# Kernel optimization log

Hardware: AMD Instinct MI355X
Metric: run time of the kernel (lower is better)

## Reference

```python
import jax, jax.numpy as jnp
from jax import lax
import numpy as np

SMOOTH = 1e-4
BN_EPS = 1e-5


def setup_inputs() -> dict:
    key = jax.random.key(0)
    k0, k1, k2, k3 = jax.random.split(key, 4)
    B, C, H, W = 8, 256, 32, 32
    heads, head_dim = 8, 64
    inner = heads * head_dim
    x = jax.random.normal(k0, (B, C, H, W), jnp.float32)
    w_qkv = jax.random.normal(k1, (3 * inner, C, 3, 3), jnp.float32) * 0.02
    head_scale = jax.random.normal(k2, (heads,), jnp.float32)
    w_out = jax.random.normal(k3, (C, inner, 1, 1), jnp.float32) * 0.05
    gamma = jnp.ones((C,), jnp.float32)
    beta = jnp.zeros((C,), jnp.float32)
    return {"x": x, "w_qkv": w_qkv, "head_scale": head_scale,
            "w_out": w_out, "gamma": gamma, "beta": beta}


def _relative_pos_dis(H, W):
    yy, xx = jnp.meshgrid(jnp.arange(H), jnp.arange(W), indexing="ij")
    y = yy.reshape(-1).astype(jnp.float32)
    x = xx.reshape(-1).astype(jnp.float32)
    dy = (y[:, None] - y[None, :]) / H
    dx = (x[:, None] - x[None, :]) / W
    return dy * dy + dx * dx  # [HW, HW]


def reference(x, w_qkv, head_scale, w_out, gamma, beta):
    B, C, H, W = x.shape
    heads = head_scale.shape[0]
    N = H * W
    # qkv 3x3 conv, no bias
    qkv = lax.conv_general_dilated(x, w_qkv, (1, 1), "SAME",
                                   dimension_numbers=("NCHW", "OIHW", "NCHW"))
    inner = qkv.shape[1] // 3
    d = inner // heads
    q, k, v = jnp.split(qkv, 3, axis=1)
    # 'b (g d) h w -> b g (h w) d'
    def resh(t):
        return t.reshape(B, heads, d, N).transpose(0, 1, 3, 2)
    q, k, v = resh(q), resh(k), resh(v)
    # cosine-similarity attention (smoothed)
    attn = jnp.einsum("bgnd,bgmd->bgnm", q, k)
    qn = jnp.sqrt(jnp.sum(q * q, axis=-1) + SMOOTH)  # [B,g,N]
    kn = jnp.sqrt(jnp.sum(k * k, axis=-1) + SMOOTH)
    attn = attn / (qn[:, :, :, None] * kn[:, :, None, :] + SMOOTH)
    # learned per-head Gaussian positional bias
    s = jax.nn.sigmoid(head_scale) * (0.4 - 0.003) + 0.003
    scale_factor = 1.0 / (2.0 * s * s)  # [g]
    dis = _relative_pos_dis(H, W)  # [N,N]
    pb = jnp.exp(-scale_factor[:, None, None] * dis[None, :, :])
    pb = pb / jnp.sum(pb, axis=-1, keepdims=True)
    attn = attn * pb[None]
    out = jnp.einsum("bgnm,bgmd->bgnd", attn, v)
    # 'b g (h w) d -> b (g d) h w'
    out = out.transpose(0, 1, 3, 2).reshape(B, inner, H, W)
    # output projection: 1x1 conv + BatchNorm2d (train-mode batch stats) + ReLU
    out = lax.conv_general_dilated(out, w_out, (1, 1), "VALID",
                                   dimension_numbers=("NCHW", "OIHW", "NCHW"))
    mean = jnp.mean(out, axis=(0, 2, 3))
    var = jnp.mean((out - mean[None, :, None, None]) ** 2, axis=(0, 2, 3))
    out = (out - mean[None, :, None, None]) * (
        gamma[None, :, None, None] * lax.rsqrt(var + BN_EPS)[None, :, None, None]
    ) + beta[None, :, None, None]
    return jax.nn.relu(out)
```

## Files before the change

### kernel.cpp

```cpp
#include <hip/hip_runtime.h>
#include <math.h>

#define SMOOTH 1e-4f
#define BN_EPS 1e-5f

constexpr int Bn = 8;
constexpr int Cc = 256;
constexpr int Nn = 1024;
constexpr int G = 8;
constexpr int INNER = 512;
constexpr int OC = 1536;
constexpr int KK = 2304;

typedef unsigned short u16;
typedef __bf16 bf16x8 __attribute__((ext_vector_type(8)));
typedef float f32x4 __attribute__((ext_vector_type(4)));
typedef unsigned short us8 __attribute__((ext_vector_type(8)));
typedef unsigned short us4 __attribute__((ext_vector_type(4)));

__device__ __forceinline__ u16 f2bf(float f) {
  unsigned int u = __float_as_uint(f);
  unsigned int r = (u + 0x7fffu + ((u >> 16) & 1u)) >> 16;
  return (u16)r;
}
__device__ __forceinline__ float bf2f(u16 u) {
  return __uint_as_float(((unsigned int)u) << 16);
}

__device__ __forceinline__ float waveSum(float v) {
#pragma unroll
  for (int off = 32; off > 0; off >>= 1) v += __shfl_xor(v, off, 64);
  return v;
}

__device__ __forceinline__ void gl16(const u16* g, u16* l) {
  __builtin_amdgcn_global_load_lds(
      (const __attribute__((address_space(1))) unsigned int*)g,
      (__attribute__((address_space(3))) unsigned int*)l, 16, 0, 0);
}

__device__ __forceinline__ bf16x8 ld8(const u16* p) {
  return __builtin_bit_cast(bf16x8, *reinterpret_cast<const us8*>(p));
}

__device__ __forceinline__ void barrier_raw() {
  asm volatile("" ::: "memory");
  __builtin_amdgcn_s_barrier();
  asm volatile("" ::: "memory");
  __builtin_amdgcn_sched_barrier(0);
}

__device__ __forceinline__ bf16x8 ldfrag(const u16* base, int row, int col) {
  int idx = (row * 64 + col) ^ ((row & 7) << 3);
  return ld8(base + idx);
}

__global__ __launch_bounds__(256) void prep_kernel(
    const float* __restrict__ wq, const float* __restrict__ wout,
    const float* __restrict__ x, const float* __restrict__ head_scale,
    u16* __restrict__ wA, u16* __restrict__ wB, u16* __restrict__ xT,
    u16* __restrict__ zpage, float* __restrict__ etab,
    float* __restrict__ idn) {
  __shared__ __align__(16) char smraw[9216];
  const int bid = blockIdx.x;
  const int tid = threadIdx.x;

  if (bid < 1536) {
    float* sw = (float*)smraw;
    const int oc = bid;
    for (int i = tid; i < KK; i += 256) sw[i] = wq[(size_t)oc * KK + i];
    __syncthreads();
#pragma unroll
    for (int j = 0; j < 2; ++j) {
      int c8 = tid + j * 256;
      if (c8 < KK / 8) {
        us8 v;
#pragma unroll
        for (int e = 0; e < 8; ++e) {
          int k = c8 * 8 + e;
          int tap = k >> 8, ic = k & 255;
          v[e] = f2bf(sw[ic * 9 + tap]);
        }
        *reinterpret_cast<us8*>(wA + (size_t)oc * KK + c8 * 8) = v;
      }
    }
  } else if (bid < 1600) {
    const int idx = (bid - 1536) * 256 + tid;
    const float4 a = reinterpret_cast<const float4*>(wout)[idx * 2];
    const float4 b = reinterpret_cast<const float4*>(wout)[idx * 2 + 1];
    us8 v;
    v[0] = f2bf(a.x); v[1] = f2bf(a.y); v[2] = f2bf(a.z); v[3] = f2bf(a.w);
    v[4] = f2bf(b.x); v[5] = f2bf(b.y); v[6] = f2bf(b.z); v[7] = f2bf(b.w);
    reinterpret_cast<us8*>(wB)[idx] = v;
    if (bid == 1536) zpage[tid] = 0;
  } else if (bid < 2112) {
    u16* sxt = (u16*)smraw;
    const int lb = bid - 1600;
    const int b = lb >> 6;
    const int nt = (lb >> 1) & 31;
    const int icc = lb & 1;
    const int n0 = nt * 32;
    const int ic0 = icc * 128;
    const float* xb = x + (size_t)b * Cc * Nn;
    {
      const int px = tid & 31;
      const int ic8 = tid >> 5;
#pragma unroll
      for (int i2 = 0; i2 < 16; ++i2) {
        const int ic = ic8 * 16 + i2;
        sxt[px * 136 + ic] = f2bf(xb[(size_t)(ic0 + ic) * Nn + n0 + px]);
      }
    }
    __syncthreads();
    const int c8 = tid & 7;
    const int px = tid >> 3;
    u16* dst = xT + (((size_t)b * 1024 + n0 + px) * 256) + ic0 + c8 * 8;
#pragma unroll
    for (int c32 = 0; c32 < 2; ++c32)
      *reinterpret_cast<us8*>(dst + c32 * 64) =
          *reinterpret_cast<const us8*>(sxt + px * 136 + c32 * 64 + c8 * 8);
  } else {
    float* et = (float*)smraw;
    float* rsum = (float*)smraw + 64;
    const int g = bid - 2112;
    const float hs = head_scale[g];
    const float sg = 1.f / (1.f + __expf(-hs));
    const float s = sg * (0.4f - 0.003f) + 0.003f;
    const float sf = 1.f / (2.f * s * s);
    if (tid < 64) {
      float v = 0.f;
      if (tid < 63) {
        float d = (float)(tid - 31) * (1.f / 32.f);
        v = __expf(-sf * d * d);
      }
      et[tid] = v;
      etab[g * 64 + tid] = v;
    }
    __syncthreads();
    if (tid < 32) {
      float sum = 0.f;
#pragma unroll
      for (int ym = 0; ym < 32; ++ym) sum += et[tid - ym + 31];
      rsum[tid] = sum;
    }
    __syncthreads();
    for (int i = tid; i < 1024; i += 256)
      idn[g * 1024 + i] = 1.f / (rsum[i >> 5] * rsum[i & 31]);
  }
}

__global__ __launch_bounds__(512, 1) void qkv_gemm_kernel(
    const u16* __restrict__ wA, const u16* __restrict__ xT,
    const u16* __restrict__ zpage, const float* __restrict__ idn,
    u16* __restrict__ qt, u16* __restrict__ ktp, u16* __restrict__ vt) {
  const int tid = threadIdx.x;
  const int lane = tid & 63;
  const int wv = tid >> 6;
  const int wm = wv >> 2, wn = wv & 3;
  const int h = lane >> 4, l15 = lane & 15;
  const int wgid = ((int)blockIdx.x & 7) * 32 + ((int)blockIdx.x >> 3);
  const int bm = wgid & 7;
  const int bn = wgid >> 3;
  const int m0 = bm * 192;

  __shared__ __align__(16) u16 smem[57344];

  const int arow = tid >> 3;
  const int aslot = (tid & 7) ^ (arow & 7);
  const u16* gA0 = wA + (size_t)(m0 + arow) * KK + aslot * 8;
  const int bslot8 = ((tid & 3) ^ (((tid >> 2) & 3) ^ ((tid >> 4) & 3))) * 8;
  const int pimgBase = ((bn & 3) << 8) + (tid >> 2);
  const u16* xTb = xT + (size_t)(bn >> 2) * (1024 * 256);

  auto mkSrc = [&](int tap, int pass) -> const u16* {
    const int dyq = (tap * 11) >> 5;
    const int ddx = tap - 3 * dyq - 1;
    const int ddy = dyq - 1;
    const int pimg = pimgBase + pass * 128;
    const int sx = (pimg & 31) + ddx;
    const int sy = (pimg >> 5) + ddy;
    if (((unsigned)sx < 32u) && ((unsigned)sy < 32u))
      return xTb + (size_t)(pimg + ddx + ddy * 32) * 256 + bslot8;
    return zpage;
  };
  const u16* srcB0 = mkSrc(0, 0);
  const u16* srcB1 = mkSrc(0, 1);
  int koff = 0;

  const int aX = l15 & 7;
  const int bX = (l15 & 3) ^ ((l15 >> 2) & 3);
  const u16* aBase = smem + (wm * 96 + l15) * 64;
  const u16* bBase = smem + 12288 + (wn * 64 + l15) * 32;
  const int slA0 = (h ^ aX) * 8;
  const int slA1 = ((4 + h) ^ aX) * 8;
  const int slB = (h ^ bX) * 8;

  f32x4 acc[6][4];
#pragma unroll
  for (int i = 0; i < 6; ++i)
#pragma unroll
    for (int j = 0; j < 4; ++j) acc[i][j] = (f32x4){0.f, 0.f, 0.f, 0.f};

  auto STAGE_A = [&](int pass, int dbuf, int kti) {
    gl16(gA0 + (size_t)pass * 64 * KK + kti * 64,
         smem + dbuf + pass * 4096 + tid * 8);
  };
  auto STAGE_B = [&](int kap, int pass, int dbuf) {
    gl16((pass ? srcB1 : srcB0) + koff + kap * 32,
         smem + dbuf + 12288 + kap * 8192 + pass * 4096 + tid * 8);
  };

  STAGE_A(0, 0, 0); STAGE_A(1, 0, 0); STAGE_A(2, 0, 0);
  STAGE_B(0, 0, 0); STAGE_B(0, 1, 0);
  STAGE_B(1, 0, 0); STAGE_B(1, 1, 0);
  asm volatile("s_waitcnt vmcnt(2)" ::: "memory");
  barrier_raw();

  bf16x8 af[3], bf[4];
#pragma unroll 1
  for (int kt = 0; kt < 36; ++kt) {
    const int buf = (kt & 1) * 28672;
    const int nbuf = 28672 - buf;
    const bool more = (kt < 35);

    if (more && (kt & 3) == 3) {
      const int ntap = (kt + 1) >> 2;
      srcB0 = mkSrc(ntap, 0);
      srcB1 = mkSrc(ntap, 1);
    }
    koff = ((kt + 1) & 3) << 6;

#pragma unroll
    for (int ni = 0; ni < 4; ++ni) bf[ni] = ld8(bBase + buf + ni * 512 + slB);
#pragma unroll
    for (int q = 0; q < 3; ++q) af[q] = ld8(aBase + buf + q * 1024 + slA0);
    if (more) { STAGE_A(0, nbuf, kt + 1); STAGE_A(1, nbuf, kt + 1); }
    barrier_raw();
    __builtin_amdgcn_s_setprio(1);
#pragma unroll
    for (int q = 0; q < 3; ++q)
#pragma unroll
      for (int ni = 0; ni < 4; ++ni)
        acc[q][ni] = __builtin_amdgcn_mfma_f32_16x16x32_bf16(af[q], bf[ni], acc[q][ni], 0, 0, 0);
    __builtin_amdgcn_s_setprio(0);

#pragma unroll
    for (int q = 0; q < 3; ++q) af[q] = ld8(aBase + buf + (3 + q) * 1024 + slA0);
    if (more) {
      STAGE_A(2, nbuf, kt + 1); STAGE_B(0, 0, nbuf);
      asm volatile("s_waitcnt vmcnt(4)" ::: "memory");
    } else {
      asm volatile("s_waitcnt vmcnt(0)" ::: "memory");
    }
    barrier_raw();
    __builtin_amdgcn_s_setprio(1);
#pragma unroll
    for (int q = 0; q < 3; ++q)
#pragma unroll
      for (int ni = 0; ni < 4; ++ni)
        acc[3 + q][ni] = __builtin_amdgcn_mfma_f32_16x16x32_bf16(af[q], bf[ni], acc[3 + q][ni], 0, 0, 0);
    __builtin_amdgcn_s_setprio(0);

#pragma unroll
    for (int ni = 0; ni < 4; ++ni) bf[ni] = ld8(bBase + buf + 8192 + ni * 512 + slB);
#pragma unroll
    for (int q = 0; q < 3; ++q) af[q] = ld8(aBase + buf + q * 1024 + slA1);
    if (more) { STAGE_B(0, 1, nbuf); STAGE_B(1, 0, nbuf); }
    barrier_raw();
    __builtin_amdgcn_s_setprio(1);
#pragma unroll
    for (int q = 0; q < 3; ++q)
#pragma unroll
      for (int ni = 0; ni < 4; ++ni)
        acc[q][ni] = __builtin_amdgcn_mfma_f32_16x16x32_bf16(af[q], bf[ni], acc[q][ni], 0, 0, 0);
    __builtin_amdgcn_s_setprio(0);

#pragma unroll
    for (int q = 0; q < 3; ++q) af[q] = ld8(aBase + buf + (3 + q) * 1024 + slA1);
    if (more) {
      STAGE_B(1, 1, nbuf);
      asm volatile("s_waitcnt vmcnt(2)" ::: "memory");
    }
    barrier_raw();
    __builtin_amdgcn_s_setprio(1);
#pragma unroll
    for (int q = 0; q < 3; ++q)
#pragma unroll
      for (int ni = 0; ni < 4; ++ni)
        acc[3 + q][ni] = __builtin_amdgcn_mfma_f32_16x16x32_bf16(af[q], bf[ni], acc[3 + q][ni], 0, 0, 0);
    __builtin_amdgcn_s_setprio(0);
  }

  const int b = bn >> 2;
  const int nimgBase = (bn & 3) * 256 + wn * 64;
  float ssF[4], ssH[4];
#pragma unroll
  for (int ni = 0; ni < 4; ++ni) {
    float sF = 0.f, sH = 0.f;
#pragma unroll
    for (int m4 = 0; m4 < 6; ++m4) {
      float s = 0.f;
#pragma unroll
      for (int r = 0; r < 4; ++r) s += acc[m4][ni][r] * acc[m4][ni][r];
      const bool isFull = (wm == 0) ? (m4 < 4) : (m4 >= 2);
      if (isFull) sF += s; else sH += s;
    }
    sF += __shfl_xor(sF, 16, 64); sF += __shfl_xor(sF, 32, 64);
    sH += __shfl_xor(sH, 16, 64); sH += __shfl_xor(sH, 32, 64);
    ssF[ni] = sF; ssH[ni] = sH;
  }
  float* xch = (float*)smem;
  if (h == 0) {
#pragma unroll
    for (int ni = 0; ni < 4; ++ni)
      xch[((wm * 4 + wn) * 4 + ni) * 16 + l15] = ssH[ni];
  }
  __syncthreads();
#pragma unroll
  for (int ni = 0; ni < 4; ++ni)
    ssH[ni] += xch[(((1 - wm) * 4 + wn) * 4 + ni) * 16 + l15];

  const int headF = (wm == 0) ? 3 * bm : 3 * bm + 2;
  const int headH = 3 * bm + 1;
  const int secF = headF >> 3, gF = headF & 7;
  const int secH = headH >> 3, gH = headH & 7;
  float rsF[4], rsH[4];
#pragma unroll
  for (int ni = 0; ni < 4; ++ni) {
    const int nimg = nimgBase + ni * 16 + l15;
    float rf = rsqrtf(ssF[ni] + SMOOTH);
    if (secF == 0) rf *= idn[gF * 1024 + nimg];
    rsF[ni] = rf;
    float rh = rsqrtf(ssH[ni] + SMOOTH);
    if (secH == 0) rh *= idn[gH * 1024 + nimg];
    rsH[ni] = rh;
  }
#pragma unroll
  for (int m4 = 0; m4 < 6; ++m4) {
    const bool isFull = (wm == 0) ? (m4 < 4) : (m4 >= 2);
    const int head = isFull ? headF : headH;
    const int sec = head >> 3, g = head & 7;
    const int d0 = isFull ? ((wm == 0) ? m4 * 16 : (m4 - 2) * 16)
                          : ((wm == 0) ? (m4 - 4) * 16 : 32 + m4 * 16);
    const size_t bg = (size_t)b * G + g;
    if (sec < 2) {
      u16* basep = (sec ? ktp : qt) + bg * 65536;
#pragma unroll
      for (int ni = 0; ni < 4; ++ni) {
        const float rs = isFull ? rsF[ni] : rsH[ni];
        const int nimg = nimgBase + ni * 16 + l15;
        us4 v;
        v[0] = f2bf(acc[m4][ni][0] * rs);
        v[1] = f2bf(acc[m4][ni][1] * rs);
        v[2] = f2bf(acc[m4][ni][2] * rs);
        v[3] = f2bf(acc[m4][ni][3] * rs);
        *reinterpret_cast<us4*>(basep + (size_t)nimg * 64 + d0 + 4 * h) = v;
      }
    } else {
      u16* basep = vt + bg * 65536;
#pragma unroll
      for (int ni = 0; ni < 4; ++ni) {
        const int nimg = nimgBase + ni * 16 + l15;
#pragma unroll
        for (int r = 0; r < 4; ++r)
          basep[(size_t)(d0 + 4 * h + r) * 1024 + nimg] = f2bf(acc[m4][ni][r]);
      }
    }
  }
}

__global__ __launch_bounds__(256, 2) void attn_mfma_kernel(
    const u16* __restrict__ qt, const u16* __restrict__ ktp,
    const u16* __restrict__ vt, const float* __restrict__ etab,
    u16* __restrict__ aout) {
  const int tid = threadIdx.x;
  const int lane = tid & 63;
  const int wv = tid >> 6;
  const int h = lane >> 4;
  const int l15 = lane & 15;
  const int wgid = (blockIdx.x & 7) * 64 + (blockIdx.x >> 3);
  const int g = wgid >> 6;
  const int b = (wgid >> 3) & 7;
  const int nb = wgid & 7;

  __shared__ __align__(16) u16 smem[32768];
  __shared__ float etabL[64];
  u16* sQ = smem;
  u16* sP = smem + 24576 + wv * 2048;

  const size_t bg = (size_t)b * G + g;
  const u16* qg = qt + bg * 65536;
  const u16* kg = ktp + bg * 65536;
  const u16* vg = vt + bg * 65536;

  if (tid < 64) etabL[tid] = etab[g * 64 + tid];

  const int srow = tid >> 3;
  const int scol = ((tid & 7) ^ (srow & 7)) * 8;

#pragma unroll
  for (int pass = 0; pass < 4; ++pass)
    gl16(qg + (size_t)(nb * 128 + pass * 32 + srow) * 64 + scol,
         sQ + pass * 2048 + tid * 8);
#pragma unroll
  for (int pass = 0; pass < 2; ++pass) {
    gl16(kg + (size_t)(pass * 32 + srow) * 64 + scol,
         smem + 8192 + pass * 2048 + tid * 8);
    gl16(vg + (size_t)(pass * 32 + srow) * 1024 + scol,
         smem + 16384 + pass * 2048 + tid * 8);
  }
  __syncthreads();

  const int col8 = h * 8;

  bf16x8 aq[2][2];
#pragma unroll
  for (int kk = 0; kk < 2; ++kk) {
    aq[kk][0] = ldfrag(sQ, wv * 32 + l15, kk * 32 + col8);
    aq[kk][1] = ldfrag(sQ, wv * 32 + 16 + l15, kk * 32 + col8);
  }

  float exv[2][4][2];
  int ynr[2][4];
#pragma unroll
  for (int ti = 0; ti < 2; ++ti)
#pragma unroll
    for (int r = 0; r < 4; ++r) {
      int n = nb * 128 + wv * 32 + ti * 16 + 4 * h + r;
      int xn = n & 31;
      ynr[ti][r] = n >> 5;
      exv[ti][r][0] = etabL[xn - l15 + 31];
      exv[ti][r][1] = etabL[xn - l15 + 15];
    }

  f32x4 oacc[2][4];
#pragma unroll
  for (int ti = 0; ti < 2; ++ti)
#pragma unroll
    for (int dj = 0; dj < 4; ++dj) oacc[ti][dj] = (f32x4){0.f, 0.f, 0.f, 0.f};

  for (int mt = 0; mt < 16; ++mt) {
    const u16* sKb = smem + 8192 + (mt & 1) * 4096;
    const u16* sVb = smem + 16384 + (mt & 1) * 4096;
    if (mt < 15) {
      const int nt2 = mt + 1;
      const int d = nt2 & 1;
#pragma unroll
      for (int pass = 0; pass < 2; ++pass) {
        gl16(kg + (size_t)(nt2 * 64 + pass * 32 + srow) * 64 + scol,
             smem + 8192 + d * 4096 + pass * 2048 + tid * 8);
        gl16(vg + (size_t)(pass * 32 + srow) * 1024 + nt2 * 64 + scol,
             smem + 16384 + d * 4096 + pass * 2048 + tid * 8);
      }
    }

    float eyv[2][4][2];
#pragma unroll
    for (int ti = 0; ti < 2; ++ti)
#pragma unroll
      for (int r = 0; r < 4; ++r) {
        eyv[ti][r][0] = etabL[ynr[ti][r] - 2 * mt + 31];
        eyv[ti][r][1] = etabL[ynr[ti][r] - 2 * mt + 30];
      }

    f32x4 sacc[2][4];
#pragma unroll
    for (int ti = 0; ti < 2; ++ti)
#pragma unroll
      for (int tj = 0; tj < 4; ++tj) sacc[ti][tj] = (f32x4){0.f, 0.f, 0.f, 0.f};
#pragma unroll
    for (int kk = 0; kk < 2; ++kk) {
#pragma unroll
      for (int tj = 0; tj < 4; ++tj) {
        bf16x8 bk = ldfrag(sKb, tj * 16 + l15, kk * 32 + col8);
        sacc[0][tj] = __builtin_amdgcn_mfma_f32_16x16x32_bf16(aq[kk][0], bk, sacc[0][tj], 0, 0, 0);
        sacc[1][tj] = __builtin_amdgcn_mfma_f32_16x16x32_bf16(aq[kk][1], bk, sacc[1][tj], 0, 0, 0);
      }
    }

#pragma unroll
    for (int tj = 0; tj < 4; ++tj) {
#pragma unroll
      for (int ti = 0; ti < 2; ++ti) {
#pragma unroll
        for (int r = 0; r < 4; ++r) {
          float wgt = sacc[ti][tj][r] * (eyv[ti][r][tj >> 1] * exv[ti][r][tj & 1]);
          int nl = ti * 16 + 4 * h + r;
          int pidx = (nl * 64 + tj * 16 + l15) ^ ((nl & 7) << 3);
          sP[pidx] = f2bf(wgt);
        }
      }
    }

#pragma unroll
    for (int km = 0; km < 2; ++km) {
      bf16x8 ap0 = ldfrag(sP, l15, km * 32 + col8);
      bf16x8 ap1 = ldfrag(sP, 16 + l15, km * 32 + col8);
#pragma unroll
      for (int dj = 0; dj < 4; ++dj) {
        bf16x8 bvv = ldfrag(sVb, dj * 16 + l15, km * 32 + col8);
        oacc[0][dj] = __builtin_amdgcn_mfma_f32_16x16x32_bf16(ap0, bvv, oacc[0][dj], 0, 0, 0);
        oacc[1][dj] = __builtin_amdgcn_mfma_f32_16x16x32_bf16(ap1, bvv, oacc[1][dj], 0, 0, 0);
      }
    }
    __syncthreads();
  }

  u16* sO = smem + 8192;
#pragma unroll
  for (int ti = 0; ti < 2; ++ti)
#pragma unroll
    for (int dj = 0; dj < 4; ++dj)
#pragma unroll
      for (int r = 0; r < 4; ++r) {
        int nl = wv * 32 + ti * 16 + 4 * h + r;
        int idx = (nl * 64 + dj * 16 + l15) ^ ((nl & 7) << 3);
        sO[idx] = f2bf(oacc[ti][dj][r]);
      }
  __syncthreads();
  {
    const int row = tid >> 1, c = (tid & 1) * 4;
    us8* dst = reinterpret_cast<us8*>(aout + (bg * 1024 + (size_t)nb * 128 + row) * 64);
#pragma unroll
    for (int k = 0; k < 4; ++k) {
      int idx = (row * 64 + (c + k) * 8) ^ ((row & 7) << 3);
      dst[c + k] = *reinterpret_cast<const us8*>(sO + idx);
    }
  }
}

__global__ __launch_bounds__(256, 4) void conv1x1_mfma_kernel(
    const u16* __restrict__ aout, const u16* __restrict__ wB,
    u16* __restrict__ proj, float* __restrict__ partials) {
  const int tid = threadIdx.x;
  const int lane = tid & 63;
  const int wv = tid >> 6;
  const int wr = wv >> 1, wc = wv & 1;
  const int h = lane >> 4, l15 = lane & 15;
  const int bm = blockIdx.x & 3;
  const int ntile = blockIdx.x >> 2;
  const int b = ntile >> 4;
  const int n0 = (ntile & 15) * 64;
  const int c0 = bm * 64;

  __shared__ __align__(16) u16 smem[16384];

  f32x4 acc[2][2];
#pragma unroll
  for (int i = 0; i < 2; ++i)
#pragma unroll
    for (int j = 0; j < 2; ++j) acc[i][j] = (f32x4){0.f, 0.f, 0.f, 0.f};

  const int srow = tid >> 3;
  const int scol = (tid & 7) * 8;

  auto STG = [&](int ks) {
    const int d = ks & 1;
#pragma unroll
    for (int pass = 0; pass < 2; ++pass) {
      gl16(wB + (size_t)(c0 + pass * 32 + srow) * 512 + ks * 64 + scol,
           smem + d * 4096 + pass * 2048 + tid * 8);
      gl16(aout + ((size_t)(b * G + ks) * 1024 + n0 + pass * 32 + srow) * 64 + scol,
           smem + 8192 + d * 4096 + pass * 2048 + tid * 8);
    }
  };

  STG(0);
  __syncthreads();
  for (int ks = 0; ks < 8; ++ks) {
    if (ks < 7) STG(ks + 1);
    const u16* sA = smem + (ks & 1) * 4096;
    const u16* sB = smem + 8192 + (ks & 1) * 4096;
#pragma unroll
    for (int kk = 0; kk < 2; ++kk) {
      bf16x8 af[2], bv[2];
#pragma unroll
      for (int mt = 0; mt < 2; ++mt)
        af[mt] = ld8(sA + (wr * 32 + mt * 16 + l15) * 64 + kk * 32 + h * 8);
#pragma unroll
      for (int nt = 0; nt < 2; ++nt)
        bv[nt] = ld8(sB + (wc * 32 + nt * 16 + l15) * 64 + kk * 32 + h * 8);
#pragma unroll
      for (int mt = 0; mt < 2; ++mt)
#pragma unroll
        for (int nt = 0; nt < 2; ++nt)
          acc[mt][nt] = __builtin_amdgcn_mfma_f32_16x16x32_bf16(af[mt], bv[nt], acc[mt][nt], 0, 0, 0);
    }
    __syncthreads();
  }

#pragma unroll
  for (int mt = 0; mt < 2; ++mt)
#pragma unroll
    for (int nt = 0; nt < 2; ++nt)
#pragma unroll
      for (int r = 0; r < 4; ++r) {
        const int c = c0 + wr * 32 + mt * 16 + 4 * h + r;
        const int n = n0 + wc * 32 + nt * 16 + l15;
        proj[((size_t)b * Cc + c) * Nn + n] = f2bf(acc[mt][nt][r]);
      }

  const int slab = ((b * 16 + (ntile & 15)) << 1) + wc;
#pragma unroll
  for (int mt = 0; mt < 2; ++mt)
#pragma unroll
    for (int r = 0; r < 4; ++r) {
      float s1 = acc[mt][0][r] + acc[mt][1][r];
      float s2 = acc[mt][0][r] * acc[mt][0][r] + acc[mt][1][r] * acc[mt][1][r];
#pragma unroll
      for (int o = 8; o >= 1; o >>= 1) {
        s1 += __shfl_xor(s1, o, 64);
        s2 += __shfl_xor(s2, o, 64);
      }
      if (l15 == 0) {
        const int c = c0 + wr * 32 + mt * 16 + 4 * h + r;
        partials[(size_t)c * 256 + slab] = s1;
        partials[65536 + (size_t)c * 256 + slab] = s2;
      }
    }
}

__global__ __launch_bounds__(256) void bn_reduce_kernel(
    const float* __restrict__ partials, float* __restrict__ stats) {
  const int c = blockIdx.x;
  const int tid = threadIdx.x;
  float s1 = partials[(size_t)c * 256 + tid];
  float s2 = partials[65536 + (size_t)c * 256 + tid];
  s1 = waveSum(s1);
  s2 = waveSum(s2);
  __shared__ float r1[4], r2[4];
  if ((tid & 63) == 0) { r1[tid >> 6] = s1; r2[tid >> 6] = s2; }
  __syncthreads();
  if (tid == 0) {
    float S = r1[0] + r1[1] + r1[2] + r1[3];
    float S2 = r2[0] + r2[1] + r2[2] + r2[3];
    const float invM = 1.f / (float)(Bn * Nn);
    float mean = S * invM;
    float var = S2 * invM - mean * mean;
    stats[c] = mean;
    stats[Cc + c] = rsqrtf(var + BN_EPS);
  }
}

__global__ __launch_bounds__(256) void bn_apply_kernel(
    const u16* __restrict__ proj, const float* __restrict__ stats,
    const float* __restrict__ gamma, const float* __restrict__ beta,
    float* __restrict__ out) {
  const int idx = blockIdx.x * 256 + threadIdx.x;
  const int flat = idx << 2;
  const int c = (flat >> 10) & (Cc - 1);
  us4 v = reinterpret_cast<const us4*>(proj)[idx];
  const float mean = stats[c];
  const float sc = stats[Cc + c] * gamma[c];
  const float sh = beta[c];
  float4 o;
  o.x = fmaxf((bf2f(v[0]) - mean) * sc + sh, 0.f);
  o.y = fmaxf((bf2f(v[1]) - mean) * sc + sh, 0.f);
  o.z = fmaxf((bf2f(v[2]) - mean) * sc + sh, 0.f);
  o.w = fmaxf((bf2f(v[3]) - mean) * sc + sh, 0.f);
  reinterpret_cast<float4*>(out)[idx] = o;
}

extern "C" void kernel_launch(void* const* d_in, const int* in_sizes, int n_in,
                              void* d_out, int out_size, void* d_ws, size_t ws_size,
                              hipStream_t stream) {
  const float* x = (const float*)d_in[0];
  const float* w_qkv = (const float*)d_in[1];
  const float* head_scale = (const float*)d_in[2];
  const float* w_out = (const float*)d_in[3];
  const float* gamma = (const float*)d_in[4];
  const float* beta = (const float*)d_in[5];
  float* out = (float*)d_out;

  char* w = (char*)d_ws;
  u16* qt = (u16*)(w + 0);
  u16* kt = (u16*)(w + 8388608);
  u16* vt = (u16*)(w + 16777216);
  u16* wA = (u16*)(w + 25165824);
  u16* aout = (u16*)(w + 25165824);
  u16* xT = (u16*)(w + 33554432);
  float* partials = (float*)(w + 33554432);
  u16* proj = (u16*)(w + 37748736);
  float* etab = (float*)(w + 71303168);
  float* idn = (float*)(w + 71305216);
  u16* zpage = (u16*)(w + 71337984);
  float* stats = (float*)(w + 71860224);
  u16* wB = (u16*)(w + 71862272);

  prep_kernel<<<dim3(2120), dim3(256), 0, stream>>>(
      w_qkv, w_out, x, head_scale, wA, wB, xT, zpage, etab, idn);
  qkv_gemm_kernel<<<dim3(256), dim3(512), 0, stream>>>(wA, xT, zpage, idn, qt, kt, vt);
  attn_mfma_kernel<<<dim3(512), dim3(256), 0, stream>>>(qt, kt, vt, etab, aout);
  conv1x1_mfma_kernel<<<dim3(512), dim3(256), 0, stream>>>(aout, wB, proj, partials);
  bn_reduce_kernel<<<dim3(Cc), dim3(256), 0, stream>>>(partials, stats);
  bn_apply_kernel<<<dim3((Bn * Cc * Nn / 4) / 256), dim3(256), 0, stream>>>(proj, stats, gamma, beta, out);
}
```

Measured before the change: 113.4 us.

## Halve attention query tile and compute Gaussian bias inline with exp

```diff
diff --git a/kernel.cpp b/kernel.cpp
--- a/kernel.cpp
+++ b/kernel.cpp
@@ -369,160 +369,134 @@
   }
 }
 
-__global__ __launch_bounds__(256, 2) void attn_mfma_kernel(
+__global__ __launch_bounds__(256, 4) void attn_mfma_kernel(
     const u16* __restrict__ qt, const u16* __restrict__ ktp,
-    const u16* __restrict__ vt, const float* __restrict__ etab,
+    const u16* __restrict__ vt, const float* __restrict__ head_scale,
     u16* __restrict__ aout) {
   const int tid = threadIdx.x;
   const int lane = tid & 63;
   const int wv = tid >> 6;
   const int h = lane >> 4;
   const int l15 = lane & 15;
-  const int wgid = (blockIdx.x & 7) * 64 + (blockIdx.x >> 3);
-  const int g = wgid >> 6;
-  const int b = (wgid >> 3) & 7;
-  const int nb = wgid & 7;
-
-  __shared__ __align__(16) u16 smem[32768];
-  __shared__ float etabL[64];
-  u16* sQ = smem;
-  u16* sP = smem + 24576 + wv * 2048;
+  const int wgid = (blockIdx.x & 7) * 128 + (blockIdx.x >> 3);
+  const int g = wgid >> 7;
+  const int b = (wgid >> 4) & 7;
+  const int nb = wgid & 15;
+
+  __shared__ __align__(16) u16 smem[20480];
+  u16* sP = smem + 16384 + wv * 1024;
 
   const size_t bg = (size_t)b * G + g;
   const u16* qg = qt + bg * 65536;
   const u16* kg = ktp + bg * 65536;
   const u16* vg = vt + bg * 65536;
 
-  if (tid < 64) etabL[tid] = etab[g * 64 + tid];
+  const float hs = head_scale[g];
+  const float sg = 1.f / (1.f + __expf(-hs));
+  const float sv = sg * (0.4f - 0.003f) + 0.003f;
+  const float sf = 1.f / (2.f * sv * sv);
 
   const int srow = tid >> 3;
   const int scol = ((tid & 7) ^ (srow & 7)) * 8;
 
 #pragma unroll
-  for (int pass = 0; pass < 4; ++pass)
-    gl16(qg + (size_t)(nb * 128 + pass * 32 + srow) * 64 + scol,
-         sQ + pass * 2048 + tid * 8);
-#pragma unroll
   for (int pass = 0; pass < 2; ++pass) {
     gl16(kg + (size_t)(pass * 32 + srow) * 64 + scol,
+         smem + pass * 2048 + tid * 8);
+    gl16(vg + (size_t)(pass * 32 + srow) * 1024 + scol,
          smem + 8192 + pass * 2048 + tid * 8);
-    gl16(vg + (size_t)(pass * 32 + srow) * 1024 + scol,
-         smem + 16384 + pass * 2048 + tid * 8);
-  }
+  }
+
+  const int col8 = h * 8;
+  const int nbase = nb * 64 + wv * 16;
+  bf16x8 aq[2];
+#pragma unroll
+  for (int kk = 0; kk < 2; ++kk)
+    aq[kk] = ld8(qg + (size_t)(nbase + l15) * 64 + kk * 32 + col8);
+
+  float ynr[4], xnr[4];
+#pragma unroll
+  for (int r = 0; r < 4; ++r) {
+    int n = nbase + 4 * h + r;
+    ynr[r] = (float)(n >> 5);
+    xnr[r] = (float)(n & 31);
+  }
+  const float xm0 = (float)l15, xm1 = (float)(l15 + 16);
+
+  f32x4 oacc[4];
+#pragma unroll
+  for (int dj = 0; dj < 4; ++dj) oacc[dj] = (f32x4){0.f, 0.f, 0.f, 0.f};
+
   __syncthreads();
 
-  const int col8 = h * 8;
-
-  bf16x8 aq[2][2];
-#pragma unroll
-  for (int kk = 0; kk < 2; ++kk) {
-    aq[kk][0] = ldfrag(sQ, wv * 32 + l15, kk * 32 + col8);
-    aq[kk][1] = ldfrag(sQ, wv * 32 + 16 + l15, kk * 32 + col8);
-  }
-
-  float exv[2][4][2];
-  int ynr[2][4];
-#pragma unroll
-  for (int ti = 0; ti < 2; ++ti)
-#pragma unroll
-    for (int r = 0; r < 4; ++r) {
-      int n = nb * 128 + wv * 32 + ti * 16 + 4 * h + r;
-      int xn = n & 31;
-      ynr[ti][r] = n >> 5;
-      exv[ti][r][0] = etabL[xn - l15 + 31];
-      exv[ti][r][1] = etabL[xn - l15 + 15];
-    }
-
-  f32x4 oacc[2][4];
-#pragma unroll
-  for (int ti = 0; ti < 2; ++ti)
-#pragma unroll
-    for (int dj = 0; dj < 4; ++dj) oacc[ti][dj] = (f32x4){0.f, 0.f, 0.f, 0.f};
-
   for (int mt = 0; mt < 16; ++mt) {
-    const u16* sKb = smem + 8192 + (mt & 1) * 4096;
-    const u16* sVb = smem + 16384 + (mt & 1) * 4096;
+    const u16* sKb = smem + (mt & 1) * 4096;
+    const u16* sVb = smem + 8192 + (mt & 1) * 4096;
     if (mt < 15) {
       const int nt2 = mt + 1;
       const int d = nt2 & 1;
 #pragma unroll
       for (int pass = 0; pass < 2; ++pass) {
         gl16(kg + (size_t)(nt2 * 64 + pass * 32 + srow) * 64 + scol,
+             smem + d * 4096 + pass * 2048 + tid * 8);
+        gl16(vg + (size_t)(pass * 32 + srow) * 1024 + nt2 * 64 + scol,
              smem + 8192 + d * 4096 + pass * 2048 + tid * 8);
-        gl16(vg + (size_t)(pass * 32 + srow) * 1024 + nt2 * 64 + scol,
-             smem + 16384 + d * 4096 + pass * 2048 + tid * 8);
-      }
-    }
-
-    float eyv[2][4][2];
-#pragma unroll
-    for (int ti = 0; ti < 2; ++ti)
-#pragma unroll
-      for (int r = 0; r < 4; ++r) {
-        eyv[ti][r][0] = etabL[ynr[ti][r] - 2 * mt + 31];
-        eyv[ti][r][1] = etabL[ynr[ti][r] - 2 * mt + 30];
-      }
-
-    f32x4 sacc[2][4];
-#pragma unroll
-    for (int ti = 0; ti < 2; ++ti)
-#pragma unroll
-      for (int tj = 0; tj < 4; ++tj) sacc[ti][tj] = (f32x4){0.f, 0.f, 0.f, 0.f};
-#pragma unroll
-    for (int kk = 0; kk < 2; ++kk) {
+      }
+    }
+
+    f32x4 sacc[4];
+#pragma unroll
+    for (int tj = 0; tj < 4; ++tj) sacc[tj] = (f32x4){0.f, 0.f, 0.f, 0.f};
+#pragma unroll
+    for (int kk = 0; kk < 2; ++kk)
 #pragma unroll
       for (int tj = 0; tj < 4; ++tj) {
         bf16x8 bk = ldfrag(sKb, tj * 16 + l15, kk * 32 + col8);
-        sacc[0][tj] = __builtin_amdgcn_mfma_f32_16x16x32_bf16(aq[kk][0], bk, sacc[0][tj], 0, 0, 0);
-        sacc[1][tj] = __builtin_amdgcn_mfma_f32_16x16x32_bf16(aq[kk][1], bk, sacc[1][tj], 0, 0, 0);
-      }
-    }
+        sacc[tj] = __builtin_amdgcn_mfma_f32_16x16x32_bf16(aq[kk], bk, sacc[tj], 0, 0, 0);
+      }
 
 #pragma unroll
     for (int tj = 0; tj < 4; ++tj) {
-#pragma unroll
-      for (int ti = 0; ti < 2; ++ti) {
-#pragma unroll
-        for (int r = 0; r < 4; ++r) {
-          float wgt = sacc[ti][tj][r] * (eyv[ti][r][tj >> 1] * exv[ti][r][tj & 1]);
-          int nl = ti * 16 + 4 * h + r;
-          int pidx = (nl * 64 + tj * 16 + l15) ^ ((nl & 7) << 3);
-          sP[pidx] = f2bf(wgt);
-        }
+      const float ymf = (float)(2 * mt + (tj >> 1));
+      const float xmf = (tj & 1) ? xm1 : xm0;
+#pragma unroll
+      for (int r = 0; r < 4; ++r) {
+        float dy = (ynr[r] - ymf) * (1.f / 32.f);
+        float dx = (xnr[r] - xmf) * (1.f / 32.f);
+        float wgt = sacc[tj][r] * __expf(-sf * (dy * dy + dx * dx));
+        int nl = 4 * h + r;
+        int pidx = (nl * 64 + tj * 16 + l15) ^ ((nl & 7) << 3);
+        sP[pidx] = f2bf(wgt);
       }
     }
 
 #pragma unroll
     for (int km = 0; km < 2; ++km) {
-      bf16x8 ap0 = ldfrag(sP, l15, km * 32 + col8);
-      bf16x8 ap1 = ldfrag(sP, 16 + l15, km * 32 + col8);
+      bf16x8 ap = ldfrag(sP, l15, km * 32 + col8);
 #pragma unroll
       for (int dj = 0; dj < 4; ++dj) {
         bf16x8 bvv = ldfrag(sVb, dj * 16 + l15, km * 32 + col8);
-        oacc[0][dj] = __builtin_amdgcn_mfma_f32_16x16x32_bf16(ap0, bvv, oacc[0][dj], 0, 0, 0);
-        oacc[1][dj] = __builtin_amdgcn_mfma_f32_16x16x32_bf16(ap1, bvv, oacc[1][dj], 0, 0, 0);
+        oacc[dj] = __builtin_amdgcn_mfma_f32_16x16x32_bf16(ap, bvv, oacc[dj], 0, 0, 0);
       }
     }
     __syncthreads();
   }
 
-  u16* sO = smem + 8192;
-#pragma unroll
-  for (int ti = 0; ti < 2; ++ti)
-#pragma unroll
-    for (int dj = 0; dj < 4; ++dj)
-#pragma unroll
-      for (int r = 0; r < 4; ++r) {
-        int nl = wv * 32 + ti * 16 + 4 * h + r;
-        int idx = (nl * 64 + dj * 16 + l15) ^ ((nl & 7) << 3);
-        sO[idx] = f2bf(oacc[ti][dj][r]);
-      }
+  u16* sO = smem;
+#pragma unroll
+  for (int dj = 0; dj < 4; ++dj)
+#pragma unroll
+    for (int r = 0; r < 4; ++r) {
+      int nl = wv * 16 + 4 * h + r;
+      int idx = (nl * 64 + dj * 16 + l15) ^ ((nl & 7) << 3);
+      sO[idx] = f2bf(oacc[dj][r]);
+    }
   __syncthreads();
   {
-    const int row = tid >> 1, c = (tid & 1) * 4;
-    us8* dst = reinterpret_cast<us8*>(aout + (bg * 1024 + (size_t)nb * 128 + row) * 64);
-#pragma unroll
-    for (int k = 0; k < 4; ++k) {
+    const int row = tid >> 2, c = (tid & 3) * 2;
+    us8* dst = reinterpret_cast<us8*>(aout + (bg * 1024 + (size_t)nb * 64 + row) * 64);
+#pragma unroll
+    for (int k = 0; k < 2; ++k) {
       int idx = (row * 64 + (c + k) * 8) ^ ((row & 7) << 3);
       dst[c + k] = *reinterpret_cast<const us8*>(sO + idx);
     }
@@ -690,7 +664,7 @@
   prep_kernel<<<dim3(2120), dim3(256), 0, stream>>>(
       w_qkv, w_out, x, head_scale, wA, wB, xT, zpage, etab, idn);
   qkv_gemm_kernel<<<dim3(256), dim3(512), 0, stream>>>(wA, xT, zpage, idn, qt, kt, vt);
-  attn_mfma_kernel<<<dim3(512), dim3(256), 0, stream>>>(qt, kt, vt, etab, aout);
+  attn_mfma_kernel<<<dim3(1024), dim3(256), 0, stream>>>(qt, kt, vt, head_scale, aout);
   conv1x1_mfma_kernel<<<dim3(512), dim3(256), 0, stream>>>(aout, wB, proj, partials);
   bn_reduce_kernel<<<dim3(Cc), dim3(256), 0, stream>>>(partials, stats);
   bn_apply_kernel<<<dim3((Bn * Cc * Nn / 4) / 256), dim3(256), 0, stream>>>(proj, stats, gamma, beta, out);
```

Result: slower. 117.6 us (+3.7%).
